# Kernel optimization log

Measured on AMD Instinct MI355X. Metric: run time of the kernel, lower is better.

## Reference

```python
import jax, jax.numpy as jnp
import numpy as np

N_NODES = 50000


def _gcn_conv(x, row, col, W, b, n_nodes):
    # symmetric-norm GCN conv with self loops already appended to (row, col)
    deg = jax.ops.segment_sum(jnp.ones_like(row, dtype=x.dtype), row, num_segments=n_nodes)
    # every node has a self loop, so deg >= 1; pow(-0.5) is finite
    dis = deg ** -0.5
    norm = dis[row] * dis[col]                       # [E']
    msg = x[row] * norm[:, None]                     # gather + scale  [E', d]
    agg = jax.ops.segment_sum(msg, col, num_segments=n_nodes)  # scatter-add [N, d]
    return agg @ W + b


def setup_inputs() -> dict:
    key = jax.random.key(0)
    ks = jax.random.split(key, 12)
    N, E, Q, d_in, h = N_NODES, 800000, 200000, 64, 128
    x = jax.random.normal(ks[0], (N, d_in), dtype=jnp.float32)
    edge_index = jax.random.randint(ks[1], (2, E), 0, N)
    edge_label_index = jax.random.randint(ks[2], (2, Q), 0, N)
    def lin(k, fan_in, fan_out):
        kw, kb = jax.random.split(k)
        bound = 1.0 / np.sqrt(fan_in)
        W = jax.random.uniform(kw, (fan_in, fan_out), minval=-bound, maxval=bound, dtype=jnp.float32)
        b = jax.random.uniform(kb, (fan_out,), minval=-bound, maxval=bound, dtype=jnp.float32)
        return W, b
    W1, b1 = lin(ks[3], d_in, h)
    W2, b2 = lin(ks[4], h, h)
    Wc1, bc1 = lin(ks[5], 2 * h, h)
    Wc2, bc2 = lin(ks[6], h, 1)
    return {"x": x, "edge_index": edge_index, "edge_label_index": edge_label_index,
            "W1": W1, "b1": b1, "W2": W2, "b2": b2,
            "Wc1": Wc1, "bc1": bc1, "Wc2": Wc2, "bc2": bc2}


def reference(x, edge_index, edge_label_index, W1, b1, W2, b2, Wc1, bc1, Wc2, bc2):
    n = x.shape[0]
    loops = jnp.arange(n, dtype=edge_index.dtype)
    row = jnp.concatenate([edge_index[0], loops])
    col = jnp.concatenate([edge_index[1], loops])
    h1 = jax.nn.relu(_gcn_conv(x, row, col, W1, b1, n))
    h2 = _gcn_conv(h1, row, col, W2, b2, n)
    src, dst = edge_label_index[0], edge_label_index[1]
    h = jnp.concatenate([h2[src], h2[dst]], axis=1)  # [Q, 2*hidden]
    h = jax.nn.relu(h @ Wc1 + bc1)
    return h @ Wc2 + bc2                              # [Q, 1]
```

## Files before the change

### kernel.cpp

```cpp
#include <hip/hip_runtime.h>


#define HB 64
#define NWIN 16384

typedef __attribute__((ext_vector_type(8))) short short8;
typedef __attribute__((ext_vector_type(4))) float floatx4;

static __device__ __forceinline__ unsigned int f2bf(float v) {
    union { float f; unsigned int u; } c; c.f = v;
    unsigned int lsb = (c.u >> 16) & 1u;
    c.u += 0x7FFFu + lsb;
    return c.u >> 16;
}
static __device__ __forceinline__ float bf2f(unsigned int h) {
    union { float f; unsigned int u; } c; c.u = h << 16;
    return c.f;
}

__global__ __launch_bounds__(256) void k_pre(const int* __restrict__ row,
                                             const int* __restrict__ col,
                                             unsigned int* __restrict__ hRow,
                                             unsigned int* __restrict__ hCol,
                                             const float* __restrict__ x,
                                             unsigned int* __restrict__ xb,
                                             const float* __restrict__ W1,
                                             const float* __restrict__ W2,
                                             const float* __restrict__ Wc1,
                                             const float* __restrict__ b2,
                                             const float* __restrict__ bc1,
                                             unsigned short* __restrict__ UVhi,
                                             unsigned short* __restrict__ UVlo,
                                             unsigned short* __restrict__ W1hi,
                                             unsigned short* __restrict__ W1lo,
                                             float* __restrict__ buv,
                                             int E, int N, int W, int chunk,
                                             int nHist, int nXb) {
    __shared__ unsigned int lds[NWIN];
    int t = threadIdx.x, b = blockIdx.x;
    if (b < nHist) {
        int hb = b % HB;
        int yb = b / HB;
        int p = yb >> 1, win = yb & 1;
        int base = win * NWIN;
        int wcap = min(W - base, NWIN);
        if (wcap <= 0) return;
        const int* idxArr = p ? col : row;
        unsigned int* outArr = p ? hCol : hRow;
        int e0 = hb * chunk, e1 = min(E, e0 + chunk);
        for (int i = t; i < wcap; i += 256) lds[i] = 0;
        __syncthreads();
        for (int e = e0 + t; e < e1; e += 256) {
            int idx = idxArr[e];
            int w = (idx >> 1) - base;
            if ((unsigned)w < (unsigned)wcap)
                atomicAdd(&lds[w], 1u << ((idx & 1) * 16));
        }
        __syncthreads();
        for (int i = t; i < wcap; i += 256)
            outArr[(size_t)hb * W + base + i] = lds[i];
    } else if (b < nHist + nXb) {
        int i = (b - nHist) * 256 + t;
        if (i < N * 32) {
            float2 v = ((const float2*)x)[i];
            xb[i] = f2bf(v.x) | (f2bf(v.y) << 16);
        }
    } else {
        int bf = b - nHist - nXb;
        float* w2row = (float*)lds;
        if (bf < 128) {
            int k = bf;
            int j = t & 127, half = t >> 7;
            int n = half * 128 + j;
            const float* wc = Wc1 + (size_t)half * 128 * 128 + j;
            if (t < 128) w2row[t] = W2[k * 128 + t];
            __syncthreads();
            float acc = 0.f;
#pragma unroll 8
            for (int m = 0; m < 128; m++) acc += w2row[m] * wc[(size_t)m * 128];
            int kstep = k >> 5, kl = k & 31, quad = kl >> 3, j8 = kl & 7;
            int nb = n >> 4, l = quad * 16 + (n & 15);
            int pidx = ((kstep * 16 + nb) * 64 + l) * 8 + j8;
            unsigned int h = f2bf(acc);
            UVhi[pidx] = (unsigned short)h;
            UVlo[pidx] = (unsigned short)f2bf(acc - bf2f(h));
        } else if (bf == 128) {
            int j = t & 127, half = t >> 7;
            const float* wc = Wc1 + (size_t)half * 128 * 128 + j;
            float acc = half ? 0.f : bc1[j];
#pragma unroll 8
            for (int m = 0; m < 128; m++) acc += b2[m] * wc[(size_t)m * 128];
            buv[half * 128 + j] = acc;
        } else {
            int idx = (bf - 129) * 256 + t;
            int k = idx >> 7, n = idx & 127;
            float v = W1[k * 128 + n];
            int kstep = k >> 5, kl = k & 31, quad = kl >> 3, j8 = kl & 7;
            int nb = n >> 4, l = quad * 16 + (n & 15);
            int pidx = ((kstep * 8 + nb) * 64 + l) * 8 + j8;
            unsigned int h = f2bf(v);
            W1hi[pidx] = (unsigned short)h;
            W1lo[pidx] = (unsigned short)f2bf(v - bf2f(h));
        }
    }
}

__global__ __launch_bounds__(256) void k_rs(const unsigned int* __restrict__ hRow,
                                            unsigned int* __restrict__ hCol,
                                            float* __restrict__ dis,
                                            int* __restrict__ offs,
                                            int* __restrict__ bsum,
                                            int N, int W) {
    __shared__ int ts[256];
    int t = threadIdx.x;
    int w = blockIdx.x * 256 + t;
    unsigned int r0 = 0, r1 = 0, c0 = 0, c1 = 0;
    if (w < W) {
#pragma unroll 8
        for (int b = 0; b < HB; b++) {
            size_t idx = (size_t)b * W + w;
            unsigned int hr = hRow[idx];
            unsigned int hc = hCol[idx];
            hCol[idx] = c0 | (c1 << 16);
            r0 += hr & 0xFFFFu; r1 += hr >> 16;
            c0 += hc & 0xFFFFu; c1 += hc >> 16;
        }
        int n0 = 2 * w, n1 = 2 * w + 1;
        dis[n0] = 1.0f / sqrtf((float)(r0 + 1));
        if (n1 < N) dis[n1] = 1.0f / sqrtf((float)(r1 + 1));
    }
    int sum = (w < W) ? (int)(c0 + c1) : 0;
    ts[t] = sum;
    __syncthreads();
    for (int off = 1; off < 256; off <<= 1) {
        int xv = (t >= off) ? ts[t - off] : 0;
        __syncthreads();
        ts[t] += xv;
        __syncthreads();
    }
    int e = ts[t] - sum;
    if (w < W) {
        int n0 = 2 * w, n1 = 2 * w + 1;
        offs[n0] = e;
        if (n1 < N) offs[n1] = e + (int)c0;
    }
    if (t == 255) bsum[blockIdx.x] = ts[255];
}

__global__ __launch_bounds__(256) void k_scan2(int* __restrict__ bsum, int B) {
    __shared__ int ts[256];
    int t = threadIdx.x;
    int v = (t < B) ? bsum[t] : 0;
    ts[t] = v;
    __syncthreads();
    for (int off = 1; off < 256; off <<= 1) {
        int x = (t >= off) ? ts[t - off] : 0;
        __syncthreads();
        ts[t] += x;
        __syncthreads();
    }
    if (t < B) bsum[t] = ts[t] - v;
}

__global__ __launch_bounds__(256) void k_scan3(int* __restrict__ offs,
                                               const int* __restrict__ bsum,
                                               int N, int E) {
    int i = blockIdx.x * 256 + threadIdx.x;
    if (i < N) offs[i] = offs[i] + bsum[i >> 9];
    if (i == 0) offs[N] = E;
}

__global__ __launch_bounds__(256) void k_fill3(const int* __restrict__ row,
                                               const int* __restrict__ col,
                                               const int* __restrict__ offs,
                                               const unsigned int* __restrict__ hCol,
                                               int* __restrict__ srcSorted,
                                               int E, int N, int W, int chunk) {
    __shared__ int base[NWIN];
    int t = threadIdx.x, b = blockIdx.x;
    int n0 = blockIdx.y * NWIN;
    int nCnt = min(NWIN, N - n0);
    int e0 = b * chunk, e1 = min(E, e0 + chunk);
    for (int wl = t; wl * 2 < nCnt; wl += 256) {
        unsigned int pref = hCol[(size_t)b * W + (n0 >> 1) + wl];
        int nn = n0 + wl * 2;
        base[wl * 2] = offs[nn] + (int)(pref & 0xFFFFu);
        if (wl * 2 + 1 < nCnt)
            base[wl * 2 + 1] = offs[nn + 1] + (int)(pref >> 16);
    }
    __syncthreads();
    for (int e = e0 + t; e < e1; e += 256) {
        int c = col[e] - n0;
        if ((unsigned)c < (unsigned)nCnt) {
            int pos = atomicAdd(&base[c], 1);
            srcSorted[pos] = row[e];
        }
    }
}

__global__ __launch_bounds__(256) void k_conv1(const unsigned short* __restrict__ s,
                                               const int* __restrict__ offs,
                                               const int* __restrict__ srcs,
                                               const float* __restrict__ dis,
                                               const unsigned short* __restrict__ Bhi,
                                               const unsigned short* __restrict__ Blo,
                                               const float* __restrict__ b1,
                                               unsigned short* __restrict__ h1b, int N) {
    __shared__ unsigned short Ahi[16][72];
    __shared__ unsigned short Alo[16][72];
    int t = threadIdx.x;
    int lane = t & 63, wave = t >> 6;
    int quad = lane >> 4;
    short8 bh[2][2], bl[2][2];
#pragma unroll
    for (int ks = 0; ks < 2; ks++)
#pragma unroll
        for (int nt = 0; nt < 2; nt++) {
            int nb = wave * 2 + nt;
            bh[ks][nt] = *(const short8*)(Bhi + ((ks * 8 + nb) * 64 + lane) * 8);
            bl[ks][nt] = *(const short8*)(Blo + ((ks * 8 + nb) * 64 + lane) * 8);
        }
    {
        int nl = t >> 4;
        int node = blockIdx.x * 16 + nl;
        if (node < N) {
            int c4 = (t & 15) * 4;
            int e = offs[node], eEnd = offs[node + 1];
            float dn = dis[node];
            uint2 w = *(const uint2*)(s + (size_t)node * 64 + c4);
            float4 acc;
            acc.x = bf2f(w.x & 0xFFFF) * dn; acc.y = bf2f(w.x >> 16) * dn;
            acc.z = bf2f(w.y & 0xFFFF) * dn; acc.w = bf2f(w.y >> 16) * dn;
            while (e + 1 < eEnd) {
                int sA = srcs[e], sB = srcs[e + 1];
                float dA = dis[sA], dB = dis[sB];
                uint2 vA = *(const uint2*)(s + (size_t)sA * 64 + c4);
                uint2 vB = *(const uint2*)(s + (size_t)sB * 64 + c4);
                acc.x += bf2f(vA.x & 0xFFFF) * dA + bf2f(vB.x & 0xFFFF) * dB;
                acc.y += bf2f(vA.x >> 16) * dA + bf2f(vB.x >> 16) * dB;
                acc.z += bf2f(vA.y & 0xFFFF) * dA + bf2f(vB.y & 0xFFFF) * dB;
                acc.w += bf2f(vA.y >> 16) * dA + bf2f(vB.y >> 16) * dB;
                e += 2;
            }
            if (e < eEnd) {
                int sA = srcs[e];
                float dA = dis[sA];
                uint2 vA = *(const uint2*)(s + (size_t)sA * 64 + c4);
                acc.x += bf2f(vA.x & 0xFFFF) * dA; acc.y += bf2f(vA.x >> 16) * dA;
                acc.z += bf2f(vA.y & 0xFFFF) * dA; acc.w += bf2f(vA.y >> 16) * dA;
            }
            acc.x *= dn; acc.y *= dn; acc.z *= dn; acc.w *= dn;
            unsigned int h0 = f2bf(acc.x), h1 = f2bf(acc.y),
                         h2 = f2bf(acc.z), h3 = f2bf(acc.w);
            uint2 hw; hw.x = h0 | (h1 << 16); hw.y = h2 | (h3 << 16);
            uint2 lw;
            lw.x = f2bf(acc.x - bf2f(h0)) | (f2bf(acc.y - bf2f(h1)) << 16);
            lw.y = f2bf(acc.z - bf2f(h2)) | (f2bf(acc.w - bf2f(h3)) << 16);
            *(uint2*)(&Ahi[nl][c4]) = hw;
            *(uint2*)(&Alo[nl][c4]) = lw;
        }
    }
    __syncthreads();
    int ml = lane & 15;
    floatx4 acc[2] = {};
#pragma unroll
    for (int ks = 0; ks < 2; ks++) {
        short8 ahi = *(const short8*)(&Ahi[ml][ks * 32 + quad * 8]);
        short8 alo = *(const short8*)(&Alo[ml][ks * 32 + quad * 8]);
#pragma unroll
        for (int nt = 0; nt < 2; nt++) {
            acc[nt] = __builtin_amdgcn_mfma_f32_16x16x32_bf16(ahi, bh[ks][nt], acc[nt], 0, 0, 0);
            acc[nt] = __builtin_amdgcn_mfma_f32_16x16x32_bf16(ahi, bl[ks][nt], acc[nt], 0, 0, 0);
            acc[nt] = __builtin_amdgcn_mfma_f32_16x16x32_bf16(alo, bh[ks][nt], acc[nt], 0, 0, 0);
        }
    }
    int md = blockIdx.x * 16 + quad * 4;
#pragma unroll
    for (int nt = 0; nt < 2; nt++) {
        int n0 = (wave * 2 + nt) * 16 + (lane & 15);
        float bias = b1[n0];
#pragma unroll
        for (int r = 0; r < 4; r++) {
            int node = md + r;
            if (node < N)
                h1b[(size_t)node * 128 + n0] =
                    (unsigned short)f2bf(fmaxf(acc[nt][r] + bias, 0.f) * dis[node]);
        }
    }
}

__global__ __launch_bounds__(256) void k_gather2(const unsigned short* __restrict__ s,
                                                 const int* __restrict__ offs,
                                                 const int* __restrict__ srcs,
                                                 const float* __restrict__ dis,
                                                 unsigned short* __restrict__ agg,
                                                 int N) {
    int tid = blockIdx.x * 256 + threadIdx.x;
    int node = tid >> 4;
    if (node >= N) return;
    int c8 = (tid & 15) * 8;
    int e = offs[node], eEnd = offs[node + 1];
    float dn = dis[node];
    uint4 w = *(const uint4*)(s + (size_t)node * 128 + c8);
    float a0 = bf2f(w.x & 0xFFFF), a1 = bf2f(w.x >> 16);
    float a2 = bf2f(w.y & 0xFFFF), a3 = bf2f(w.y >> 16);
    float a4 = bf2f(w.z & 0xFFFF), a5 = bf2f(w.z >> 16);
    float a6 = bf2f(w.w & 0xFFFF), a7 = bf2f(w.w >> 16);
    while (e + 1 < eEnd) {
        int sA = srcs[e], sB = srcs[e + 1];
        uint4 vA = *(const uint4*)(s + (size_t)sA * 128 + c8);
        uint4 vB = *(const uint4*)(s + (size_t)sB * 128 + c8);
        a0 += bf2f(vA.x & 0xFFFF) + bf2f(vB.x & 0xFFFF);
        a1 += bf2f(vA.x >> 16) + bf2f(vB.x >> 16);
        a2 += bf2f(vA.y & 0xFFFF) + bf2f(vB.y & 0xFFFF);
        a3 += bf2f(vA.y >> 16) + bf2f(vB.y >> 16);
        a4 += bf2f(vA.z & 0xFFFF) + bf2f(vB.z & 0xFFFF);
        a5 += bf2f(vA.z >> 16) + bf2f(vB.z >> 16);
        a6 += bf2f(vA.w & 0xFFFF) + bf2f(vB.w & 0xFFFF);
        a7 += bf2f(vA.w >> 16) + bf2f(vB.w >> 16);
        e += 2;
    }
    if (e < eEnd) {
        int sA = srcs[e];
        uint4 vA = *(const uint4*)(s + (size_t)sA * 128 + c8);
        a0 += bf2f(vA.x & 0xFFFF); a1 += bf2f(vA.x >> 16);
        a2 += bf2f(vA.y & 0xFFFF); a3 += bf2f(vA.y >> 16);
        a4 += bf2f(vA.z & 0xFFFF); a5 += bf2f(vA.z >> 16);
        a6 += bf2f(vA.w & 0xFFFF); a7 += bf2f(vA.w >> 16);
    }
    uint4 o;
    o.x = f2bf(a0 * dn) | (f2bf(a1 * dn) << 16);
    o.y = f2bf(a2 * dn) | (f2bf(a3 * dn) << 16);
    o.z = f2bf(a4 * dn) | (f2bf(a5 * dn) << 16);
    o.w = f2bf(a6 * dn) | (f2bf(a7 * dn) << 16);
    *(uint4*)(agg + (size_t)node * 128 + c8) = o;
}

__global__ __launch_bounds__(256) void k_mfmaUV(const unsigned short* __restrict__ A,
                                                const unsigned short* __restrict__ Bhi,
                                                const unsigned short* __restrict__ Blo,
                                                const float* __restrict__ buv,
                                                unsigned short* __restrict__ Ub,
                                                unsigned short* __restrict__ Vb, int N) {
    int lane = threadIdx.x & 63, wave = threadIdx.x >> 6;
    int quad = lane >> 4;
    short8 bh[4][4], bl[4][4];
#pragma unroll
    for (int ks = 0; ks < 4; ks++)
#pragma unroll
        for (int nt = 0; nt < 4; nt++) {
            int nb = wave * 4 + nt;
            bh[ks][nt] = *(const short8*)(Bhi + ((ks * 16 + nb) * 64 + lane) * 8);
            bl[ks][nt] = *(const short8*)(Blo + ((ks * 16 + nb) * 64 + lane) * 8);
        }
#pragma unroll
    for (int g = 0; g < 4; g++) {
        int mbase = blockIdx.x * 64 + g * 16;
        int ma = mbase + (lane & 15); if (ma >= N) ma = N - 1;
        floatx4 acc[4] = {};
#pragma unroll
        for (int ks = 0; ks < 4; ks++) {
            short8 a = *(const short8*)(A + (size_t)ma * 128 + ks * 32 + quad * 8);
#pragma unroll
            for (int nt = 0; nt < 4; nt++) {
                acc[nt] = __builtin_amdgcn_mfma_f32_16x16x32_bf16(a, bh[ks][nt], acc[nt], 0, 0, 0);
                acc[nt] = __builtin_amdgcn_mfma_f32_16x16x32_bf16(a, bl[ks][nt], acc[nt], 0, 0, 0);
            }
        }
        int md = mbase + quad * 4;
#pragma unroll
        for (int nt = 0; nt < 4; nt++) {
            int n0 = wave * 64 + nt * 16 + (lane & 15);
            float bias = buv[n0];
            unsigned short* dst = (n0 < 128) ? Ub : Vb;
            int cc = n0 & 127;
#pragma unroll
            for (int r = 0; r < 4; r++) {
                int node = md + r;
                if (node < N)
                    dst[(size_t)node * 128 + cc] =
                        (unsigned short)f2bf(acc[nt][r] + bias);
            }
        }
    }
}

__global__ __launch_bounds__(256) void k_head(const unsigned short* __restrict__ Ub,
                                              const unsigned short* __restrict__ Vb,
                                              const int* __restrict__ srcA,
                                              const int* __restrict__ dstA,
                                              const float* __restrict__ Wc2,
                                              const float* __restrict__ bc2,
                                              float* __restrict__ out, int Q) {
    int t = threadIdx.x;
    int q = blockIdx.x * 16 + (t >> 4);
    if (q >= Q) return;
    int l = t & 15;
    int s = srcA[q], d = dstA[q];
    uint4 u = *(const uint4*)(Ub + (size_t)s * 128 + l * 8);
    uint4 v = *(const uint4*)(Vb + (size_t)d * 128 + l * 8);
    const float4* w = (const float4*)(Wc2 + l * 8);
    float4 w0 = w[0], w1 = w[1];
    float acc = 0.f, z;
    z = fmaxf(bf2f(u.x & 0xFFFF) + bf2f(v.x & 0xFFFF), 0.f); acc += z * w0.x;
    z = fmaxf(bf2f(u.x >> 16)    + bf2f(v.x >> 16),    0.f); acc += z * w0.y;
    z = fmaxf(bf2f(u.y & 0xFFFF) + bf2f(v.y & 0xFFFF), 0.f); acc += z * w0.z;
    z = fmaxf(bf2f(u.y >> 16)    + bf2f(v.y >> 16),    0.f); acc += z * w0.w;
    z = fmaxf(bf2f(u.z & 0xFFFF) + bf2f(v.z & 0xFFFF), 0.f); acc += z * w1.x;
    z = fmaxf(bf2f(u.z >> 16)    + bf2f(v.z >> 16),    0.f); acc += z * w1.y;
    z = fmaxf(bf2f(u.w & 0xFFFF) + bf2f(v.w & 0xFFFF), 0.f); acc += z * w1.z;
    z = fmaxf(bf2f(u.w >> 16)    + bf2f(v.w >> 16),    0.f); acc += z * w1.w;
    acc += __shfl_xor(acc, 1);
    acc += __shfl_xor(acc, 2);
    acc += __shfl_xor(acc, 4);
    acc += __shfl_xor(acc, 8);
    if (l == 0) out[q] = acc + bc2[0];
}

extern "C" void kernel_launch(void* const* d_in, const int* in_sizes, int n_in,
                              void* d_out, int out_size, void* d_ws, size_t ws_size,
                              hipStream_t stream) {
    const float* x   = (const float*)d_in[0];
    const int*   ei  = (const int*)d_in[1];
    const int*   eli = (const int*)d_in[2];
    const float* W1  = (const float*)d_in[3];
    const float* b1  = (const float*)d_in[4];
    const float* W2  = (const float*)d_in[5];
    const float* b2  = (const float*)d_in[6];
    const float* Wc1 = (const float*)d_in[7];
    const float* bc1 = (const float*)d_in[8];
    const float* Wc2 = (const float*)d_in[9];
    const float* bc2 = (const float*)d_in[10];
    float* out = (float*)d_out;
    char* wsb = (char*)d_ws;

    const int N = in_sizes[0] / 64;
    const int E = in_sizes[1] / 2;
    const int Q = in_sizes[2] / 2;
    const int W = (N + 1) / 2;
    const int chunk = (E + HB - 1) / HB;
    const int nPass = (N + NWIN - 1) / NWIN;
    const int nWinH = (W + NWIN - 1) / NWIN;
    const int nHist = HB * 2 * nWinH;
    const int nXb   = (N * 32 + 255) / 256;
    const int rsB   = (W + 255) / 256;

    float* dis       = (float*)wsb;
    int*   offs      = (int*)wsb + 65536;
    int*   bsum      = (int*)wsb + 197120;
    float* buv       = (float*)wsb + 262912;
    unsigned short* UVhi = (unsigned short*)((int*)wsb + 263168);
    unsigned short* UVlo = (unsigned short*)((int*)wsb + 279552);
    unsigned short* W1hi = (unsigned short*)((int*)wsb + 295936);
    unsigned short* W1lo = (unsigned short*)((int*)wsb + 300032);
    int*   srcSorted = (int*)wsb + 304128;
    unsigned short* Vb   = (unsigned short*)((int*)wsb + 1104128);
    unsigned short* h1b  = (unsigned short*)((int*)wsb + 4304128);
    unsigned short* agg2b= (unsigned short*)((int*)wsb + 7504128);
    unsigned short* Ub = h1b;
    unsigned int* hRow = (unsigned int*)wsb + 10704128;
    unsigned int* hCol = (unsigned int*)wsb + 12304128;
    unsigned int* xb   = (unsigned int*)wsb + 13904128;

    const int* row  = ei;
    const int* col  = ei + E;
    const int* srcA = eli;
    const int* dstA = eli + Q;

    k_pre<<<nHist + nXb + 161, 256, 0, stream>>>(
        row, col, hRow, hCol, x, xb, W1, W2, Wc1, b2, bc1,
        UVhi, UVlo, W1hi, W1lo, buv, E, N, W, chunk, nHist, nXb);
    k_rs<<<rsB, 256, 0, stream>>>(hRow, hCol, dis, offs, bsum, N, W);
    k_scan2<<<1, 256, 0, stream>>>(bsum, rsB);
    k_scan3<<<(N + 255) / 256, 256, 0, stream>>>(offs, bsum, N, E);
    k_fill3<<<dim3(HB, nPass), 256, 0, stream>>>(row, col, offs, hCol, srcSorted, E, N, W, chunk);
    k_conv1<<<(N + 15) / 16, 256, 0, stream>>>(
        (const unsigned short*)xb, offs, srcSorted, dis, W1hi, W1lo, b1, h1b, N);
    k_gather2<<<((size_t)N * 16 + 255) / 256, 256, 0, stream>>>(
        h1b, offs, srcSorted, dis, agg2b, N);
    k_mfmaUV<<<(N + 63) / 64, 256, 0, stream>>>(agg2b, UVhi, UVlo, buv, Ub, Vb, N);
    k_head<<<(Q + 15) / 16, 256, 0, stream>>>(Ub, Vb, srcA, dstA, Wc2, bc2, out, Q);
}
```

Before: 255.8 us.

## Fuse layer-2 gather with UV projection GEMM via shared-memory tile

Merges the second GCN gather kernel and the MFMA projection kernel into one kernel. Each 512-thread block aggregates 32 nodes into LDS, then eight waves run the bf16 MFMA on that tile, each wave covering 32 output columns. This removes the round trip of the aggregated bf16 buffer through global memory and one kernel launch. Ub gets its own buffer because h1b is still being read during the fused kernel. The cost is fewer rows per block, so each block reloads its weight fragments more often, and a larger block with LDS use may lower occupancy.

```diff
diff --git a/kernel.cpp b/kernel.cpp
--- a/kernel.cpp
+++ b/kernel.cpp
@@ -289,96 +289,98 @@
     }
 }
 
-__global__ __launch_bounds__(256) void k_gather2(const unsigned short* __restrict__ s,
-                                                 const int* __restrict__ offs,
-                                                 const int* __restrict__ srcs,
-                                                 const float* __restrict__ dis,
-                                                 unsigned short* __restrict__ agg,
-                                                 int N) {
-    int tid = blockIdx.x * 256 + threadIdx.x;
-    int node = tid >> 4;
-    if (node >= N) return;
-    int c8 = (tid & 15) * 8;
-    int e = offs[node], eEnd = offs[node + 1];
-    float dn = dis[node];
-    uint4 w = *(const uint4*)(s + (size_t)node * 128 + c8);
-    float a0 = bf2f(w.x & 0xFFFF), a1 = bf2f(w.x >> 16);
-    float a2 = bf2f(w.y & 0xFFFF), a3 = bf2f(w.y >> 16);
-    float a4 = bf2f(w.z & 0xFFFF), a5 = bf2f(w.z >> 16);
-    float a6 = bf2f(w.w & 0xFFFF), a7 = bf2f(w.w >> 16);
-    while (e + 1 < eEnd) {
-        int sA = srcs[e], sB = srcs[e + 1];
-        uint4 vA = *(const uint4*)(s + (size_t)sA * 128 + c8);
-        uint4 vB = *(const uint4*)(s + (size_t)sB * 128 + c8);
-        a0 += bf2f(vA.x & 0xFFFF) + bf2f(vB.x & 0xFFFF);
-        a1 += bf2f(vA.x >> 16) + bf2f(vB.x >> 16);
-        a2 += bf2f(vA.y & 0xFFFF) + bf2f(vB.y & 0xFFFF);
-        a3 += bf2f(vA.y >> 16) + bf2f(vB.y >> 16);
-        a4 += bf2f(vA.z & 0xFFFF) + bf2f(vB.z & 0xFFFF);
-        a5 += bf2f(vA.z >> 16) + bf2f(vB.z >> 16);
-        a6 += bf2f(vA.w & 0xFFFF) + bf2f(vB.w & 0xFFFF);
-        a7 += bf2f(vA.w >> 16) + bf2f(vB.w >> 16);
-        e += 2;
-    }
-    if (e < eEnd) {
-        int sA = srcs[e];
-        uint4 vA = *(const uint4*)(s + (size_t)sA * 128 + c8);
-        a0 += bf2f(vA.x & 0xFFFF); a1 += bf2f(vA.x >> 16);
-        a2 += bf2f(vA.y & 0xFFFF); a3 += bf2f(vA.y >> 16);
-        a4 += bf2f(vA.z & 0xFFFF); a5 += bf2f(vA.z >> 16);
-        a6 += bf2f(vA.w & 0xFFFF); a7 += bf2f(vA.w >> 16);
-    }
-    uint4 o;
-    o.x = f2bf(a0 * dn) | (f2bf(a1 * dn) << 16);
-    o.y = f2bf(a2 * dn) | (f2bf(a3 * dn) << 16);
-    o.z = f2bf(a4 * dn) | (f2bf(a5 * dn) << 16);
-    o.w = f2bf(a6 * dn) | (f2bf(a7 * dn) << 16);
-    *(uint4*)(agg + (size_t)node * 128 + c8) = o;
-}
-
-__global__ __launch_bounds__(256) void k_mfmaUV(const unsigned short* __restrict__ A,
-                                                const unsigned short* __restrict__ Bhi,
-                                                const unsigned short* __restrict__ Blo,
-                                                const float* __restrict__ buv,
-                                                unsigned short* __restrict__ Ub,
-                                                unsigned short* __restrict__ Vb, int N) {
-    int lane = threadIdx.x & 63, wave = threadIdx.x >> 6;
-    int quad = lane >> 4;
-    short8 bh[4][4], bl[4][4];
+__global__ __launch_bounds__(512) void k_conv2(const unsigned short* __restrict__ s,
+                                               const int* __restrict__ offs,
+                                               const int* __restrict__ srcs,
+                                               const float* __restrict__ dis,
+                                               const unsigned short* __restrict__ Bhi,
+                                               const unsigned short* __restrict__ Blo,
+                                               const float* __restrict__ buv,
+                                               unsigned short* __restrict__ Ub,
+                                               unsigned short* __restrict__ Vb, int N) {
+    __shared__ unsigned short Ab[32][136];
+    int t = threadIdx.x;
+    {
+        int nl = t >> 4;
+        int node = blockIdx.x * 32 + nl;
+        int c8 = (t & 15) * 8;
+        if (node < N) {
+            int e = offs[node], eEnd = offs[node + 1];
+            float dn = dis[node];
+            uint4 w = *(const uint4*)(s + (size_t)node * 128 + c8);
+            float a0 = bf2f(w.x & 0xFFFF), a1 = bf2f(w.x >> 16);
+            float a2 = bf2f(w.y & 0xFFFF), a3 = bf2f(w.y >> 16);
+            float a4 = bf2f(w.z & 0xFFFF), a5 = bf2f(w.z >> 16);
+            float a6 = bf2f(w.w & 0xFFFF), a7 = bf2f(w.w >> 16);
+            while (e + 1 < eEnd) {
+                int sA = srcs[e], sB = srcs[e + 1];
+                uint4 vA = *(const uint4*)(s + (size_t)sA * 128 + c8);
+                uint4 vB = *(const uint4*)(s + (size_t)sB * 128 + c8);
+                a0 += bf2f(vA.x & 0xFFFF) + bf2f(vB.x & 0xFFFF);
+                a1 += bf2f(vA.x >> 16) + bf2f(vB.x >> 16);
+                a2 += bf2f(vA.y & 0xFFFF) + bf2f(vB.y & 0xFFFF);
+                a3 += bf2f(vA.y >> 16) + bf2f(vB.y >> 16);
+                a4 += bf2f(vA.z & 0xFFFF) + bf2f(vB.z & 0xFFFF);
+                a5 += bf2f(vA.z >> 16) + bf2f(vB.z >> 16);
+                a6 += bf2f(vA.w & 0xFFFF) + bf2f(vB.w & 0xFFFF);
+                a7 += bf2f(vA.w >> 16) + bf2f(vB.w >> 16);
+                e += 2;
+            }
+            if (e < eEnd) {
+                int sA = srcs[e];
+                uint4 vA = *(const uint4*)(s + (size_t)sA * 128 + c8);
+                a0 += bf2f(vA.x & 0xFFFF); a1 += bf2f(vA.x >> 16);
+                a2 += bf2f(vA.y & 0xFFFF); a3 += bf2f(vA.y >> 16);
+                a4 += bf2f(vA.z & 0xFFFF); a5 += bf2f(vA.z >> 16);
+                a6 += bf2f(vA.w & 0xFFFF); a7 += bf2f(vA.w >> 16);
+            }
+            uint4 o;
+            o.x = f2bf(a0 * dn) | (f2bf(a1 * dn) << 16);
+            o.y = f2bf(a2 * dn) | (f2bf(a3 * dn) << 16);
+            o.z = f2bf(a4 * dn) | (f2bf(a5 * dn) << 16);
+            o.w = f2bf(a6 * dn) | (f2bf(a7 * dn) << 16);
+            *(uint4*)(&Ab[nl][c8]) = o;
+        } else {
+            uint4 z; z.x = 0; z.y = 0; z.z = 0; z.w = 0;
+            *(uint4*)(&Ab[nl][c8]) = z;
+        }
+    }
+    int lane = t & 63, wave = t >> 6, quad = lane >> 4, ml = lane & 15;
+    short8 bh[4][2], bl[4][2];
 #pragma unroll
     for (int ks = 0; ks < 4; ks++)
 #pragma unroll
-        for (int nt = 0; nt < 4; nt++) {
-            int nb = wave * 4 + nt;
+        for (int nt = 0; nt < 2; nt++) {
+            int nb = wave * 2 + nt;
             bh[ks][nt] = *(const short8*)(Bhi + ((ks * 16 + nb) * 64 + lane) * 8);
             bl[ks][nt] = *(const short8*)(Blo + ((ks * 16 + nb) * 64 + lane) * 8);
         }
-#pragma unroll
-    for (int g = 0; g < 4; g++) {
-        int mbase = blockIdx.x * 64 + g * 16;
-        int ma = mbase + (lane & 15); if (ma >= N) ma = N - 1;
-        floatx4 acc[4] = {};
+    __syncthreads();
+#pragma unroll
+    for (int g = 0; g < 2; g++) {
+        int mbase = blockIdx.x * 32 + g * 16;
+        floatx4 acc[2] = {};
 #pragma unroll
         for (int ks = 0; ks < 4; ks++) {
-            short8 a = *(const short8*)(A + (size_t)ma * 128 + ks * 32 + quad * 8);
-#pragma unroll
-            for (int nt = 0; nt < 4; nt++) {
+            short8 a = *(const short8*)(&Ab[g * 16 + ml][ks * 32 + quad * 8]);
+#pragma unroll
+            for (int nt = 0; nt < 2; nt++) {
                 acc[nt] = __builtin_amdgcn_mfma_f32_16x16x32_bf16(a, bh[ks][nt], acc[nt], 0, 0, 0);
                 acc[nt] = __builtin_amdgcn_mfma_f32_16x16x32_bf16(a, bl[ks][nt], acc[nt], 0, 0, 0);
             }
         }
         int md = mbase + quad * 4;
 #pragma unroll
-        for (int nt = 0; nt < 4; nt++) {
-            int n0 = wave * 64 + nt * 16 + (lane & 15);
+        for (int nt = 0; nt < 2; nt++) {
+            int n0 = (wave * 2 + nt) * 16 + ml;
             float bias = buv[n0];
             unsigned short* dst = (n0 < 128) ? Ub : Vb;
             int cc = n0 & 127;
 #pragma unroll
             for (int r = 0; r < 4; r++) {
-                int node = md + r;
-                if (node < N)
-                    dst[(size_t)node * 128 + cc] =
+                int nd = md + r;
+                if (nd < N)
+                    dst[(size_t)nd * 128 + cc] =
                         (unsigned short)f2bf(acc[nt][r] + bias);
             }
         }
@@ -456,8 +458,7 @@
     int*   srcSorted = (int*)wsb + 304128;
     unsigned short* Vb   = (unsigned short*)((int*)wsb + 1104128);
     unsigned short* h1b  = (unsigned short*)((int*)wsb + 4304128);
-    unsigned short* agg2b= (unsigned short*)((int*)wsb + 7504128);
-    unsigned short* Ub = h1b;
+    unsigned short* Ub   = (unsigned short*)((int*)wsb + 7504128);
     unsigned int* hRow = (unsigned int*)wsb + 10704128;
     unsigned int* hCol = (unsigned int*)wsb + 12304128;
     unsigned int* xb   = (unsigned int*)wsb + 13904128;
@@ -476,8 +477,7 @@
     k_fill3<<<dim3(HB, nPass), 256, 0, stream>>>(row, col, offs, hCol, srcSorted, E, N, W, chunk);
     k_conv1<<<(N + 15) / 16, 256, 0, stream>>>(
         (const unsigned short*)xb, offs, srcSorted, dis, W1hi, W1lo, b1, h1b, N);
-    k_gather2<<<((size_t)N * 16 + 255) / 256, 256, 0, stream>>>(
-        h1b, offs, srcSorted, dis, agg2b, N);
-    k_mfmaUV<<<(N + 63) / 64, 256, 0, stream>>>(agg2b, UVhi, UVlo, buv, Ub, Vb, N);
+    k_conv2<<<(N + 31) / 32, 512, 0, stream>>>(
+        h1b, offs, srcSorted, dis, UVhi, UVlo, buv, Ub, Vb, N);
     k_head<<<(Q + 15) / 16, 256, 0, stream>>>(Ub, Vb, srcA, dstA, Wc2, bc2, out, Q);
 }
```

Result: no change. 257.9 us (+0.8%).
